# Kernel optimization log

Hardware: AMD Instinct MI355X
Metric: run time of the kernel (lower is better)

## Reference

```python
import jax, jax.numpy as jnp
import numpy as np

NUM_RING = 16
MAX_RING = 1520
EPS = 1e-5


def setup_inputs() -> dict:
    key = jax.random.key(0)
    B, C, N = 16, 64, 16384
    cnt = N // NUM_RING  # 1024 points per ring, sorted
    k1, k2, k3, k4, k5 = jax.random.split(key, 5)
    x = jax.random.normal(k1, (B, C, N), dtype=jnp.float32)
    # ring ids: sorted, exactly cnt points per ring (the module assumes sorted,
    # identical-count rings across batch)
    ring = jnp.broadcast_to(jnp.arange(N, dtype=jnp.int64) // cnt, (B, N))
    # random-upsample indices: concat(arange(cnt), randperm(cnt)[:MAX_RING-cnt])
    rng = np.random.default_rng(0)
    up = MAX_RING - cnt  # 496
    choice = np.empty((B, NUM_RING, MAX_RING), dtype=np.int64)
    for b in range(B):
        for r in range(NUM_RING):
            choice[b, r, :cnt] = np.arange(cnt)
            choice[b, r, cnt:] = rng.permutation(cnt)[:up]
    choice = jnp.asarray(choice)
    # grouped Conv1d(64 -> 128, kernel 1, groups=16): weight [128, 4, 1] -> [16, 8, 4]
    Wg = jax.random.normal(k2, (NUM_RING, 8, 4), dtype=jnp.float32) * 0.5
    bias = jax.random.normal(k3, (128,), dtype=jnp.float32) * 0.1
    gamma = jnp.ones((128,), dtype=jnp.float32)
    beta = jnp.zeros((128,), dtype=jnp.float32)
    return {"x": x, "Wg": Wg, "bias": bias, "gamma": gamma, "beta": beta,
            "ring": ring, "choice": choice}


def reference(x, Wg, bias, gamma, beta, ring, choice):
    B, C, N = x.shape  # C = 64
    R, MR = NUM_RING, MAX_RING
    cnt = N // R
    L = R * MR  # 24320

    xt = jnp.transpose(x, (0, 2, 1))  # [B, N, 64]
    # per-ring gather with random upsample to MAX_RING points
    idx = (jnp.arange(R, dtype=choice.dtype)[None, :, None] * cnt + choice)  # [B,R,MR]
    gathered = jnp.take_along_axis(xt, idx.reshape(B, L, 1), axis=1)  # [B, L, 64]

    # faithful to torch: cat(...).view(B, 64, -1) is a raw reshape (channel-scrambling)
    xc = gathered.reshape(B, C, L)  # [B, 64, L]

    # grouped 1x1 conv: 16 groups, 4 in / 8 out channels each
    xg = xc.reshape(B, R, 4, L)
    y = jnp.einsum('goc,bgcl->bgol', Wg, xg).reshape(B, 128, L)
    y = y + bias[None, :, None]

    # BatchNorm1d (training mode: batch statistics, biased variance)
    mean = jnp.mean(y, axis=(0, 2))
    var = jnp.var(y, axis=(0, 2))
    y = gamma[None, :, None] * (y - mean[None, :, None]) * jax.lax.rsqrt(var + EPS)[None, :, None] + beta[None, :, None]

    # per-ring max over MAX_RING slots, broadcast back to original ring sizes
    pooled = jnp.max(y.reshape(B, 128, R, MR), axis=-1)  # [B, 128, R]
    out = jnp.repeat(pooled, cnt, axis=2)  # [B, 128, N]
    return out
```

## Files before the change

kernel.cpp:

```cpp
#include <hip/hip_runtime.h>
#include <float.h>

#define NB    16
#define CIN   64
#define NPT   16384
#define NRING 16
#define MAXR  1520
#define LTOT  (NRING*MAXR)
#define MBLK  380
#define NCH   128
#define NBLK1 (NB*CIN*2)
#define IDXS  500

typedef float fx4 __attribute__((ext_vector_type(4)));

__device__ __forceinline__ float sload(float v) {
    return __int_as_float(__builtin_amdgcn_readfirstlane(__float_as_int(v)));
}

__global__ __launch_bounds__(512) void k1_gather_conv(
    const float* __restrict__ x, const float* __restrict__ Wg,
    const float* __restrict__ bias, const float* __restrict__ gamma,
    const int* __restrict__ choice,
    float* __restrict__ p_sum, float* __restrict__ p_sqs,
    float* __restrict__ p_max)
{
    __shared__ float xs[8192];
    __shared__ unsigned short ilds[8*IDXS];

    const int blk = blockIdx.x;
    const int b  = blk >> 7;
    const int cp = (blk >> 1) & 63;
    const int h  = blk & 1;
    const int t  = threadIdx.x;

    {
        const float4* src = (const float4*)(x + ((size_t)(b*CIN + cp)) * NPT + h*8192);
        float4* dst = (float4*)xs;
        #pragma unroll
        for (int i = 0; i < 4; ++i) dst[t + i*512] = src[t + i*512];
    }
    {
        #pragma unroll
        for (int i = 0; i < 2; ++i) {
            const int J  = t + i*512;
            const int gg = J >> 7;
            const int j  = J & 127;
            if (j < 124) {
                const int4 v = *(const int4*)(choice + ((size_t)(b*NRING + h*8 + gg))*MAXR + 1024 + j*4);
                ushort4 u;
                u.x = (unsigned short)v.x; u.y = (unsigned short)v.y;
                u.z = (unsigned short)v.z; u.w = (unsigned short)v.w;
                *(ushort4*)(ilds + gg*IDXS + j*4) = u;
            }
        }
    }
    __syncthreads();

    const int g8   = t >> 6;
    const int lane = t & 63;
    const int r    = lane >> 2;
    const int s    = lane & 3;
    const int g    = h*8 + g8;

    float w[8][4], bs[8];
    #pragma unroll
    for (int o = 0; o < 8; ++o) {
        const int ch = g*8 + o;
        const float sg = (gamma[ch] < 0.0f) ? -1.0f : 1.0f;
        bs[o] = sload(sg * bias[ch]);
        #pragma unroll
        for (int c = 0; c < 4; ++c) w[o][c] = sload(sg * Wg[ch*4 + c]);
    }

    const int mlo = (r*MAXR - cp + 63) >> 6;
    int mhi = ((r+1)*MAXR - cp + 63) >> 6;
    if (mhi > MBLK) mhi = MBLK;

    const float* __restrict__ xg = xs + (g8 << 10);
    const unsigned short* __restrict__ ig = ilds + g8*IDXS;

    float smax[8], ssum[8], ssq[8];
    #pragma unroll
    for (int o = 0; o < 8; ++o) { smax[o] = -FLT_MAX; ssum[o] = 0.f; ssq[o] = 0.f; }

    const int m0 = mlo + s;

    int ix2[5], ix3[5];
    #pragma unroll
    for (int k = 0; k < 5; ++k) {
        const int m = m0 + 4*k;
        const int off2 = (m >= 264) ? (m - 264) : 0;
        const int l2 = ig[off2];
        ix2[k] = (m < 264) ? (760 + m) : l2;
        ix3[k] = ig[116 + m];
    }
    #pragma unroll
    for (int k = 0; k < 5; ++k) {
        const int m = m0 + 4*k;
        const float v0 = xg[m];
        const float v1 = xg[380 + m];
        const float v2 = xg[ix2[k]];
        const float v3 = xg[ix3[k]];
        #pragma unroll
        for (int o = 0; o < 8; ++o) {
            float y = fmaf(w[o][0], v0, fmaf(w[o][1], v1,
                      fmaf(w[o][2], v2, fmaf(w[o][3], v3, bs[o]))));
            smax[o] = fmaxf(smax[o], y);
            ssum[o] += y;
            ssq[o]  = fmaf(y, y, ssq[o]);
        }
    }
    {
        const int m = m0 + 20;
        if (m < mhi) {
            const int off2 = (m >= 264) ? (m - 264) : 0;
            const int l2 = ig[off2];
            const int idx2 = (m < 264) ? (760 + m) : l2;
            const int idx3 = ig[116 + m];
            const float v0 = xg[m];
            const float v1 = xg[380 + m];
            const float v2 = xg[idx2];
            const float v3 = xg[idx3];
            #pragma unroll
            for (int o = 0; o < 8; ++o) {
                float y = fmaf(w[o][0], v0, fmaf(w[o][1], v1,
                          fmaf(w[o][2], v2, fmaf(w[o][3], v3, bs[o]))));
                smax[o] = fmaxf(smax[o], y);
                ssum[o] += y;
                ssq[o]  = fmaf(y, y, ssq[o]);
            }
        }
    }

    #pragma unroll
    for (int o = 0; o < 8; ++o) {
        smax[o] = fmaxf(smax[o], __shfl_xor(smax[o], 1));
        ssum[o] += __shfl_xor(ssum[o], 1);
        ssq[o]  += __shfl_xor(ssq[o], 1);
        smax[o] = fmaxf(smax[o], __shfl_xor(smax[o], 2));
        ssum[o] += __shfl_xor(ssum[o], 2);
        ssq[o]  += __shfl_xor(ssq[o], 2);
    }

    if (s == 0) {
        float* base = p_max + (((size_t)(b*64 + cp))*NRING + r)*NCH + h*64 + g8*8;
        ((float4*)base)[0] = make_float4(smax[0], smax[1], smax[2], smax[3]);
        ((float4*)base)[1] = make_float4(smax[4], smax[5], smax[6], smax[7]);
    }

    __syncthreads();
    float* redS = xs;
    float* redQ = xs + 1100;
    if (s == 0) {
        #pragma unroll
        for (int o = 0; o < 8; ++o) {
            redS[(g8*8+o)*17 + r] = ssum[o];
            redQ[(g8*8+o)*17 + r] = ssq[o];
        }
    }
    __syncthreads();
    if (t < 64) {
        float S = 0.f, Q = 0.f;
        #pragma unroll
        for (int rr = 0; rr < 16; ++rr) {
            S += redS[t*17 + rr];
            Q += redQ[t*17 + rr];
        }
        const float sg = (gamma[h*64 + t] < 0.0f) ? -1.0f : 1.0f;
        p_sum[(size_t)blk*64 + t] = sg * S;
        p_sqs[(size_t)blk*64 + t] = Q;
    }
}

__global__ __launch_bounds__(256) void k23_pool_bcast(
    const float* __restrict__ p_sum, const float* __restrict__ p_sqs,
    const float* __restrict__ p_max,
    const float* __restrict__ gamma, const float* __restrict__ beta,
    fx4* __restrict__ out)
{
    __shared__ float part[16][17];
    __shared__ float wsum[4], wsq[4];
    __shared__ float pool[16];
    const int bc = blockIdx.x;
    const int b  = bc >> 7;
    const int ch = bc & 127;
    const int t  = threadIdx.x;
    const int hh = ch >> 6, c64 = ch & 63;

    const int r = t >> 4, ck = t & 15;
    float v = -FLT_MAX;
    #pragma unroll
    for (int k = 0; k < 4; ++k) {
        const int cpi = ck*4 + k;
        v = fmaxf(v, p_max[(((size_t)(b*64 + cpi))*NRING + r)*NCH + ch]);
    }

    float S = 0.f, Q = 0.f;
    #pragma unroll
    for (int i = 0; i < 4; ++i) {
        const int jj = t + i*256;
        const int b2 = jj >> 6, cp2 = jj & 63;
        const int kb = b2*128 + cp2*2 + hh;
        S += p_sum[(size_t)kb*64 + c64];
        Q += p_sqs[(size_t)kb*64 + c64];
    }
    #pragma unroll
    for (int off = 1; off < 64; off <<= 1) {
        S += __shfl_xor(S, off);
        Q += __shfl_xor(Q, off);
    }
    part[r][ck] = v;
    if ((t & 63) == 0) { wsum[t >> 6] = S; wsq[t >> 6] = Q; }
    __syncthreads();

    if (t < 16) {
        const float inv = 1.0f / (float)((size_t)NB * LTOT);
        const float Sa = wsum[0] + wsum[1] + wsum[2] + wsum[3];
        const float Qa = wsq[0] + wsq[1] + wsq[2] + wsq[3];
        const float mean = Sa * inv;
        const float var  = Qa * inv - mean*mean;
        const float istd = rsqrtf(var + 1e-5f);
        float acc = part[t][0];
        #pragma unroll
        for (int k = 1; k < 16; ++k) acc = fmaxf(acc, part[t][k]);
        const float gm = gamma[ch];
        const float raw = (gm >= 0.0f) ? acc : -acc;
        pool[t] = gm * (raw - mean) * istd + beta[ch];
    }
    __syncthreads();

    fx4* __restrict__ dst = out + (size_t)bc * (NPT/4);
    #pragma unroll
    for (int i = 0; i < 16; ++i) {
        const int idx = t + i*256;
        const float vv = pool[idx >> 8];
        fx4 val; val.x = vv; val.y = vv; val.z = vv; val.w = vv;
        __builtin_nontemporal_store(val, &dst[idx]);
    }
}

extern "C" void kernel_launch(void* const* d_in, const int* in_sizes, int n_in,
                              void* d_out, int out_size, void* d_ws, size_t ws_size,
                              hipStream_t stream)
{
    const float* x     = (const float*)d_in[0];
    const float* Wg    = (const float*)d_in[1];
    const float* bias  = (const float*)d_in[2];
    const float* gamma = (const float*)d_in[3];
    const float* beta  = (const float*)d_in[4];
    const int* choice  = (const int*)d_in[6];

    float* p_sum = (float*)d_ws;
    float* p_sqs = p_sum + (size_t)2048*64;
    float* p_max = p_sqs + (size_t)2048*64;

    k1_gather_conv<<<NBLK1, 512, 0, stream>>>(x, Wg, bias, gamma, choice,
                                              p_sum, p_sqs, p_max);
    k23_pool_bcast<<<NB*NCH, 256, 0, stream>>>(p_sum, p_sqs, p_max,
                                               gamma, beta, (fx4*)d_out);
}
```

Measured before the change: 63.54 us.

## Split gather-conv into quarter blocks with packed per-slot gather indices

The first kernel now runs four 256-thread blocks per (batch, channel-plane) instead of two 512-thread blocks, each loading a quarter of the row and handling four groups. Gather indices for the two indirect channels are precomputed per slot and packed into one 32-bit word in LDS. This removes the per-slot branch and index arithmetic and gives more, smaller blocks for occupancy. The partial-sum layout and the reduction in the second kernel are adjusted to match. The broadcast output also switches from nontemporal to regular stores, which may change cache behaviour.

```diff
diff --git a/kernel.cpp b/kernel.cpp
--- a/kernel.cpp
+++ b/kernel.cpp
@@ -9,59 +9,55 @@
 #define LTOT  (NRING*MAXR)
 #define MBLK  380
 #define NCH   128
-#define NBLK1 (NB*CIN*2)
-#define IDXS  500
-
-typedef float fx4 __attribute__((ext_vector_type(4)));
+#define NBLK1 (NB*CIN*4)
+#define MW    380
 
 __device__ __forceinline__ float sload(float v) {
     return __int_as_float(__builtin_amdgcn_readfirstlane(__float_as_int(v)));
 }
 
-__global__ __launch_bounds__(512) void k1_gather_conv(
+__global__ __launch_bounds__(256) void k1_gather_conv(
     const float* __restrict__ x, const float* __restrict__ Wg,
     const float* __restrict__ bias, const float* __restrict__ gamma,
     const int* __restrict__ choice,
     float* __restrict__ p_sum, float* __restrict__ p_sqs,
     float* __restrict__ p_max)
 {
-    __shared__ float xs[8192];
-    __shared__ unsigned short ilds[8*IDXS];
+    __shared__ float xs[4096];
+    __shared__ int   iw[4*MW];
 
     const int blk = blockIdx.x;
-    const int b  = blk >> 7;
-    const int cp = (blk >> 1) & 63;
-    const int h  = blk & 1;
+    const int b  = blk >> 8;
+    const int cp = (blk >> 2) & 63;
+    const int q  = blk & 3;
     const int t  = threadIdx.x;
 
     {
-        const float4* src = (const float4*)(x + ((size_t)(b*CIN + cp)) * NPT + h*8192);
+        const float4* src = (const float4*)(x + ((size_t)(b*CIN + cp)) * NPT + q*4096);
         float4* dst = (float4*)xs;
         #pragma unroll
-        for (int i = 0; i < 4; ++i) dst[t + i*512] = src[t + i*512];
+        for (int i = 0; i < 4; ++i) dst[t + i*256] = src[t + i*256];
     }
     {
-        #pragma unroll
-        for (int i = 0; i < 2; ++i) {
-            const int J  = t + i*512;
-            const int gg = J >> 7;
-            const int j  = J & 127;
-            if (j < 124) {
-                const int4 v = *(const int4*)(choice + ((size_t)(b*NRING + h*8 + gg))*MAXR + 1024 + j*4);
-                ushort4 u;
-                u.x = (unsigned short)v.x; u.y = (unsigned short)v.y;
-                u.z = (unsigned short)v.z; u.w = (unsigned short)v.w;
-                *(ushort4*)(ilds + gg*IDXS + j*4) = u;
+        const int g4 = t >> 6, lane = t & 63;
+        const int* __restrict__ cg = choice + ((size_t)(b*NRING + q*4 + g4)) * MAXR;
+        #pragma unroll
+        for (int k = 0; k < 6; ++k) {
+            const int m = lane + k*64;
+            if (m < MW) {
+                const int c2 = cg[760  + m];
+                const int c3 = cg[1140 + m];
+                iw[g4*MW + m] = c2 | (c3 << 16);
             }
         }
     }
     __syncthreads();
 
-    const int g8   = t >> 6;
+    const int g4   = t >> 6;
     const int lane = t & 63;
     const int r    = lane >> 2;
     const int s    = lane & 3;
-    const int g    = h*8 + g8;
+    const int g    = q*4 + g4;
 
     float w[8][4], bs[8];
     #pragma unroll
@@ -77,8 +73,8 @@
     int mhi = ((r+1)*MAXR - cp + 63) >> 6;
     if (mhi > MBLK) mhi = MBLK;
 
-    const float* __restrict__ xg = xs + (g8 << 10);
-    const unsigned short* __restrict__ ig = ilds + g8*IDXS;
+    const float* __restrict__ xg = xs + (g4 << 10);
+    const int*   __restrict__ ig = iw + g4*MW;
 
     float smax[8], ssum[8], ssq[8];
     #pragma unroll
@@ -86,22 +82,19 @@
 
     const int m0 = mlo + s;
 
-    int ix2[5], ix3[5];
+    int wv[5];
+    #pragma unroll
+    for (int k = 0; k < 5; ++k) wv[k] = ig[m0 + 4*k];
+
     #pragma unroll
     for (int k = 0; k < 5; ++k) {
         const int m = m0 + 4*k;
-        const int off2 = (m >= 264) ? (m - 264) : 0;
-        const int l2 = ig[off2];
-        ix2[k] = (m < 264) ? (760 + m) : l2;
-        ix3[k] = ig[116 + m];
-    }
-    #pragma unroll
-    for (int k = 0; k < 5; ++k) {
-        const int m = m0 + 4*k;
+        const int i2 = wv[k] & 0xFFFF;
+        const int i3 = ((unsigned)wv[k]) >> 16;
         const float v0 = xg[m];
         const float v1 = xg[380 + m];
-        const float v2 = xg[ix2[k]];
-        const float v3 = xg[ix3[k]];
+        const float v2 = xg[i2];
+        const float v3 = xg[i3];
         #pragma unroll
         for (int o = 0; o < 8; ++o) {
             float y = fmaf(w[o][0], v0, fmaf(w[o][1], v1,
@@ -114,14 +107,13 @@
     {
         const int m = m0 + 20;
         if (m < mhi) {
-            const int off2 = (m >= 264) ? (m - 264) : 0;
-            const int l2 = ig[off2];
-            const int idx2 = (m < 264) ? (760 + m) : l2;
-            const int idx3 = ig[116 + m];
+            const int wt = ig[m];
+            const int i2 = wt & 0xFFFF;
+            const int i3 = ((unsigned)wt) >> 16;
             const float v0 = xg[m];
             const float v1 = xg[380 + m];
-            const float v2 = xg[idx2];
-            const float v3 = xg[idx3];
+            const float v2 = xg[i2];
+            const float v3 = xg[i3];
             #pragma unroll
             for (int o = 0; o < 8; ++o) {
                 float y = fmaf(w[o][0], v0, fmaf(w[o][1], v1,
@@ -144,32 +136,32 @@
     }
 
     if (s == 0) {
-        float* base = p_max + (((size_t)(b*64 + cp))*NRING + r)*NCH + h*64 + g8*8;
+        float* base = p_max + (((size_t)(b*64 + cp))*NRING + r)*NCH + q*32 + g4*8;
         ((float4*)base)[0] = make_float4(smax[0], smax[1], smax[2], smax[3]);
         ((float4*)base)[1] = make_float4(smax[4], smax[5], smax[6], smax[7]);
     }
 
     __syncthreads();
     float* redS = xs;
-    float* redQ = xs + 1100;
+    float* redQ = xs + 600;
     if (s == 0) {
         #pragma unroll
         for (int o = 0; o < 8; ++o) {
-            redS[(g8*8+o)*17 + r] = ssum[o];
-            redQ[(g8*8+o)*17 + r] = ssq[o];
-        }
-    }
-    __syncthreads();
-    if (t < 64) {
+            redS[(g4*8+o)*17 + r] = ssum[o];
+            redQ[(g4*8+o)*17 + r] = ssq[o];
+        }
+    }
+    __syncthreads();
+    if (t < 32) {
         float S = 0.f, Q = 0.f;
         #pragma unroll
         for (int rr = 0; rr < 16; ++rr) {
             S += redS[t*17 + rr];
             Q += redQ[t*17 + rr];
         }
-        const float sg = (gamma[h*64 + t] < 0.0f) ? -1.0f : 1.0f;
-        p_sum[(size_t)blk*64 + t] = sg * S;
-        p_sqs[(size_t)blk*64 + t] = Q;
+        const float sg = (gamma[q*32 + t] < 0.0f) ? -1.0f : 1.0f;
+        p_sum[(size_t)blk*32 + t] = sg * S;
+        p_sqs[(size_t)blk*32 + t] = Q;
     }
 }
 
@@ -177,7 +169,7 @@
     const float* __restrict__ p_sum, const float* __restrict__ p_sqs,
     const float* __restrict__ p_max,
     const float* __restrict__ gamma, const float* __restrict__ beta,
-    fx4* __restrict__ out)
+    float4* __restrict__ out)
 {
     __shared__ float part[16][17];
     __shared__ float wsum[4], wsq[4];
@@ -186,7 +178,7 @@
     const int b  = bc >> 7;
     const int ch = bc & 127;
     const int t  = threadIdx.x;
-    const int hh = ch >> 6, c64 = ch & 63;
+    const int q  = ch >> 5, c32 = ch & 31;
 
     const int r = t >> 4, ck = t & 15;
     float v = -FLT_MAX;
@@ -201,9 +193,9 @@
     for (int i = 0; i < 4; ++i) {
         const int jj = t + i*256;
         const int b2 = jj >> 6, cp2 = jj & 63;
-        const int kb = b2*128 + cp2*2 + hh;
-        S += p_sum[(size_t)kb*64 + c64];
-        Q += p_sqs[(size_t)kb*64 + c64];
+        const int kb = ((b2*64 + cp2) << 2) | q;
+        S += p_sum[(size_t)kb*32 + c32];
+        Q += p_sqs[(size_t)kb*32 + c32];
     }
     #pragma unroll
     for (int off = 1; off < 64; off <<= 1) {
@@ -230,13 +222,12 @@
     }
     __syncthreads();
 
-    fx4* __restrict__ dst = out + (size_t)bc * (NPT/4);
+    float4* __restrict__ dst = out + (size_t)bc * (NPT/4);
     #pragma unroll
     for (int i = 0; i < 16; ++i) {
         const int idx = t + i*256;
         const float vv = pool[idx >> 8];
-        fx4 val; val.x = vv; val.y = vv; val.z = vv; val.w = vv;
-        __builtin_nontemporal_store(val, &dst[idx]);
+        dst[idx] = make_float4(vv, vv, vv, vv);
     }
 }
 
@@ -252,11 +243,11 @@
     const int* choice  = (const int*)d_in[6];
 
     float* p_sum = (float*)d_ws;
-    float* p_sqs = p_sum + (size_t)2048*64;
-    float* p_max = p_sqs + (size_t)2048*64;
-
-    k1_gather_conv<<<NBLK1, 512, 0, stream>>>(x, Wg, bias, gamma, choice,
+    float* p_sqs = p_sum + (size_t)NBLK1*32;
+    float* p_max = p_sqs + (size_t)NBLK1*32;
+
+    k1_gather_conv<<<NBLK1, 256, 0, stream>>>(x, Wg, bias, gamma, choice,
                                               p_sum, p_sqs, p_max);
     k23_pool_bcast<<<NB*NCH, 256, 0, stream>>>(p_sum, p_sqs, p_max,
-                                               gamma, beta, (fx4*)d_out);
-}
+                                               gamma, beta, (float4*)d_out);
+}
```

New measurement: 66.39 us. 4.5% more time.
